# Kernel tuning notes

Measured on AMD Instinct MI355X. Metric: run time of the kernel, lower is better.

The kernel has to match this reference:

```python
import jax, jax.numpy as jnp
import numpy as np

N_TOKENS = 8192
D_MODEL = 1024
D_FF = 4096
N_EXPERTS = 8


def setup_inputs() -> dict:
    key = jax.random.key(0)
    ks = jax.random.split(key, 5)
    scale_in = 1.0 / np.sqrt(D_MODEL)
    x = jax.random.normal(ks[0], (N_TOKENS, D_MODEL), dtype=jnp.float32)
    gate_w = jax.random.normal(ks[1], (D_MODEL, N_EXPERTS), dtype=jnp.float32) * scale_in
    gate_b = jnp.zeros((N_EXPERTS,), dtype=jnp.float32)
    expert_w = jax.random.normal(ks[2], (N_EXPERTS, D_MODEL, D_FF), dtype=jnp.float32) * scale_in
    expert_b = jnp.zeros((N_EXPERTS, D_FF), dtype=jnp.float32)
    return {"x": x, "gate_w": gate_w, "gate_b": gate_b, "expert_w": expert_w, "expert_b": expert_b}


def reference(x, gate_w, gate_b, expert_w, expert_b):
    # Gate: [N, E] logits -> softmax -> top-1 expert per token
    gate_logits = x @ gate_w + gate_b
    gate_probs = jax.nn.softmax(gate_logits, axis=-1)
    top1 = jnp.argmax(gate_probs, axis=-1)  # [N], == argsort(...)[:, -1]

    # Dense all-expert compute, as in the original: [E, N, d_ff]
    expert_outputs = jnp.einsum('nd,edf->enf', x, expert_w) + expert_b[:, None, :]

    # Gather each token's top-1 expert output: [N, d_ff]
    selected = expert_outputs[top1, jnp.arange(x.shape[0])]
    return selected
```

## Files before the change

### kernel.cpp

```cpp
#include <hip/hip_runtime.h>


#define N_TOKENS 8192
#define D_MODEL  1024
#define D_FF     4096
#define N_EXPERTS 8

#define BM 128
#define BN 128
#define BK 64
#define NKT (D_MODEL / BK)
#define MT_MAX (N_TOKENS / BM + N_EXPERTS)
#define NTILES (D_FF / BN)
#define GATE_BLOCKS (N_TOKENS / 4)
#define WCONV_BLOCKS ((D_FF / 64) * (D_MODEL / 64) * N_EXPERTS)

typedef float  floatx4 __attribute__((ext_vector_type(4)));
typedef short  short8  __attribute__((ext_vector_type(8)));

__device__ __forceinline__ unsigned short f2bf(float f) {
    union { float f; unsigned u; } a; a.f = f;
    return (unsigned short)((a.u + 0x7fffu + ((a.u >> 16) & 1u)) >> 16);
}

#define GLDS(gp, lp) __builtin_amdgcn_global_load_lds( \
    (const __attribute__((address_space(1))) unsigned int*)(const void*)(gp), \
    (__attribute__((address_space(3))) unsigned int*)(void*)(lp), 16, 0, 0)

#define WST 68
__global__ __launch_bounds__(256) void prep_kernel(
    const float* __restrict__ x, const float* __restrict__ gw,
    const float* __restrict__ gb, const float* __restrict__ ew,
    unsigned short* __restrict__ xb, unsigned short* __restrict__ wt,
    int* __restrict__ top1)
{
    if (blockIdx.x < GATE_BLOCKS) {
        int wave = threadIdx.x >> 6;
        int l    = threadIdx.x & 63;
        int n = blockIdx.x * 4 + wave;
        const float4* xr = (const float4*)(x + (size_t)n * D_MODEL);
        float acc[N_EXPERTS];
#pragma unroll
        for (int e = 0; e < N_EXPERTS; ++e) acc[e] = 0.f;
#pragma unroll
        for (int j = 0; j < 4; ++j) {
            int d4 = j * 64 + l;
            float4 v = xr[d4];
            float vv[4] = { v.x, v.y, v.z, v.w };
#pragma unroll
            for (int t = 0; t < 4; ++t) {
                const float4* g = (const float4*)(gw + (size_t)(d4 * 4 + t) * N_EXPERTS);
                float4 g0 = g[0], g1 = g[1];
                acc[0] += vv[t] * g0.x; acc[1] += vv[t] * g0.y;
                acc[2] += vv[t] * g0.z; acc[3] += vv[t] * g0.w;
                acc[4] += vv[t] * g1.x; acc[5] += vv[t] * g1.y;
                acc[6] += vv[t] * g1.z; acc[7] += vv[t] * g1.w;
            }
            union { unsigned short us[4]; uint2 u; } pk;
            pk.us[0] = f2bf(v.x); pk.us[1] = f2bf(v.y);
            pk.us[2] = f2bf(v.z); pk.us[3] = f2bf(v.w);
            ((uint2*)(xb + (size_t)n * D_MODEL))[d4] = pk.u;
        }
#pragma unroll
        for (int e = 0; e < N_EXPERTS; ++e)
            for (int off = 32; off > 0; off >>= 1)
                acc[e] += __shfl_down(acc[e], off);
        if (l == 0) {
            float best = acc[0] + gb[0]; int be = 0;
#pragma unroll
            for (int e = 1; e < N_EXPERTS; ++e) {
                float v = acc[e] + gb[e];
                if (v > best) { best = v; be = e; }
            }
            top1[n] = be;
        }
    } else {
        __shared__ unsigned short tt[64 * WST];
        int b  = blockIdx.x - GATE_BLOCKS;
        int f0 = (b & 63) * 64;
        int d0 = ((b >> 6) & 15) * 64;
        int e  = b >> 10;
        int t  = threadIdx.x;
        const float* we = ew + (size_t)e * D_MODEL * D_FF + (size_t)d0 * D_FF + f0;
        int fg = (t & 15) * 4;
        int dg = (t >> 4) * 4;
        unsigned short v[4][4];
#pragma unroll
        for (int j = 0; j < 4; ++j) {
            float4 r = *(const float4*)(we + (size_t)(dg + j) * D_FF + fg);
            v[0][j] = f2bf(r.x); v[1][j] = f2bf(r.y);
            v[2][j] = f2bf(r.z); v[3][j] = f2bf(r.w);
        }
#pragma unroll
        for (int i = 0; i < 4; ++i) {
            union { unsigned short us[4]; uint2 u; } pk;
            pk.us[0] = v[i][0]; pk.us[1] = v[i][1];
            pk.us[2] = v[i][2]; pk.us[3] = v[i][3];
            *(uint2*)&tt[(fg + i) * WST + dg] = pk.u;
        }
        __syncthreads();
        unsigned short* wte = wt + (size_t)e * D_FF * D_MODEL + (size_t)f0 * D_MODEL + d0;
        int fr = t >> 3;
        int dr = (t & 7) * 8;
#pragma unroll
        for (int p = 0; p < 2; ++p) {
            int f = fr + p * 32;
            uint2 a = *(const uint2*)&tt[f * WST + dr];
            uint2 c = *(const uint2*)&tt[f * WST + dr + 4];
            uint4 o; o.x = a.x; o.y = a.y; o.z = c.x; o.w = c.y;
            *(uint4*)(wte + (size_t)f * D_MODEL + dr) = o;
        }
    }
}

__global__ __launch_bounds__(1024) void route_kernel(
    const int* __restrict__ top1, int* __restrict__ tile_expert, int* __restrict__ list)
{
    __shared__ int wtot[16][N_EXPERTS];
    __shared__ int wbase[16][N_EXPERTS];
    __shared__ int pofs[N_EXPERTS];
    int t = threadIdx.x, wv = t >> 6, l = t & 63;

    for (int i = t; i < MT_MAX * BM; i += 1024) list[i] = -1;

    int e8[8];
    const int4* tp = (const int4*)(top1 + t * 8);
    int4 a = tp[0], b = tp[1];
    e8[0] = a.x; e8[1] = a.y; e8[2] = a.z; e8[3] = a.w;
    e8[4] = b.x; e8[5] = b.y; e8[6] = b.z; e8[7] = b.w;
    int c[N_EXPERTS], s[N_EXPERTS];
#pragma unroll
    for (int e = 0; e < N_EXPERTS; ++e) c[e] = 0;
#pragma unroll
    for (int j = 0; j < 8; ++j) c[e8[j]]++;
#pragma unroll
    for (int e = 0; e < N_EXPERTS; ++e) s[e] = c[e];
    for (int off = 1; off < 64; off <<= 1) {
#pragma unroll
        for (int e = 0; e < N_EXPERTS; ++e) {
            int v = __shfl_up(s[e], off);
            if (l >= off) s[e] += v;
        }
    }
    if (l == 63)
#pragma unroll
        for (int e = 0; e < N_EXPERTS; ++e) wtot[wv][e] = s[e];
    __syncthreads();
    if (t == 0) {
        int cnt[N_EXPERTS];
        for (int e = 0; e < N_EXPERTS; ++e) {
            cnt[e] = 0;
            for (int w = 0; w < 16; ++w) { wbase[w][e] = cnt[e]; cnt[e] += wtot[w][e]; }
        }
        int off = 0;
        for (int e = 0; e < N_EXPERTS; ++e) {
            pofs[e] = off;
            int ntl = (cnt[e] + BM - 1) / BM;
            for (int k = 0; k < ntl; ++k) tile_expert[off / BM + k] = e;
            off += ntl * BM;
        }
        for (int k = off / BM; k < MT_MAX; ++k) tile_expert[k] = -1;
    }
    __syncthreads();
    int base[N_EXPERTS];
#pragma unroll
    for (int e = 0; e < N_EXPERTS; ++e) base[e] = pofs[e] + wbase[wv][e] + s[e] - c[e];
#pragma unroll
    for (int j = 0; j < 8; ++j) {
        int e = e8[j];
        list[base[e]++] = t * 8 + j;
    }
}

__global__ __launch_bounds__(256) void gemm_kernel(
    const unsigned short* __restrict__ xb,
    const unsigned short* __restrict__ wt,
    const float* __restrict__ eb,
    const int* __restrict__ tile_expert,
    const int* __restrict__ list,
    float* __restrict__ out)
{
    int bid = blockIdx.x;
    int xcd = bid & 7, w = bid >> 3;
    int mt  = w >> 2;
    int nt  = (xcd << 2) | (w & 3);
    int e = tile_expert[mt];
    if (e < 0) return;
    int n0 = nt * BN;

    __shared__ unsigned short As[BM * BK];
    __shared__ unsigned short Bs[BN * BK];
    __shared__ int toks[BM];

    int tid = threadIdx.x;
    int lane = tid & 63, wave = tid >> 6;
    if (tid < BM) toks[tid] = list[mt * BM + tid];
    __syncthreads();

    const unsigned short* gA[4];
    const unsigned short* gB[4];
    const unsigned short* wbase = wt + (size_t)e * D_FF * D_MODEL;
#pragma unroll
    for (int i = 0; i < 4; ++i) {
        int s = wave * 256 + i * 64 + lane;
        int row = s >> 3, c8 = (s & 7) ^ (row & 7);
        int ta = toks[row]; if (ta < 0) ta = 0;
        gA[i] = xb + (size_t)ta * D_MODEL + c8 * 8;
        gB[i] = wbase + (size_t)(n0 + row) * D_MODEL + c8 * 8;
    }

    floatx4 acc[4][4];
#pragma unroll
    for (int mi = 0; mi < 4; ++mi)
#pragma unroll
        for (int ni = 0; ni < 4; ++ni)
            acc[mi][ni] = (floatx4){0.f, 0.f, 0.f, 0.f};

    int mw = (wave >> 1) * 64;
    int nw = (wave & 1) * 64;
    int q = lane >> 4, r = lane & 15;
    int xr = r & 7;
    int ra[4], rb[4];
#pragma unroll
    for (int i = 0; i < 4; ++i) { ra[i] = (mw + i * 16 + r) * 8; rb[i] = (nw + i * 16 + r) * 8; }

    for (int kt = 0; kt < NKT; ++kt) {
        int k0 = kt * BK;
#pragma unroll
        for (int i = 0; i < 4; ++i) GLDS(gA[i] + k0, &As[(wave * 256 + i * 64) * 8]);
#pragma unroll
        for (int i = 0; i < 4; ++i) GLDS(gB[i] + k0, &Bs[(wave * 256 + i * 64) * 8]);
        __syncthreads();
#pragma unroll
        for (int ks = 0; ks < 2; ++ks) {
            int cq = (ks * 4 + q) ^ xr;
            short8 af[4], bf[4];
#pragma unroll
            for (int mi = 0; mi < 4; ++mi)
                af[mi] = *(const short8*)&As[(ra[mi] + cq) * 8];
#pragma unroll
            for (int ni = 0; ni < 4; ++ni)
                bf[ni] = *(const short8*)&Bs[(rb[ni] + cq) * 8];
#pragma unroll
            for (int mi = 0; mi < 4; ++mi)
#pragma unroll
                for (int ni = 0; ni < 4; ++ni)
                    acc[mi][ni] = __builtin_amdgcn_mfma_f32_16x16x32_bf16(
                        af[mi], bf[ni], acc[mi][ni], 0, 0, 0);
        }
        __syncthreads();
    }

#pragma unroll
    for (int ni = 0; ni < 4; ++ni) {
        int f = n0 + nw + ni * 16 + r;
        float bias = eb[(size_t)e * D_FF + f];
#pragma unroll
        for (int mi = 0; mi < 4; ++mi) {
            int mbase = mw + mi * 16 + q * 4;
#pragma unroll
            for (int i = 0; i < 4; ++i) {
                int tok = toks[mbase + i];
                if (tok >= 0) out[(size_t)tok * D_FF + f] = acc[mi][ni][i] + bias;
            }
        }
    }
}

extern "C" void kernel_launch(void* const* d_in, const int* in_sizes, int n_in,
                              void* d_out, int out_size, void* d_ws, size_t ws_size,
                              hipStream_t stream) {
    const float* x  = (const float*)d_in[0];
    const float* gw = (const float*)d_in[1];
    const float* gb = (const float*)d_in[2];
    const float* ew = (const float*)d_in[3];
    const float* eb = (const float*)d_in[4];
    float* out = (float*)d_out;

    char* ws = (char*)d_ws;
    int* top1        = (int*)ws;
    int* tile_expert = (int*)(ws + 32768);
    int* list        = (int*)(ws + 36864);
    unsigned short* xb = (unsigned short*)(ws + 131072);
    unsigned short* wt = (unsigned short*)(ws + 131072 + (size_t)N_TOKENS * D_MODEL * 2);

    hipLaunchKernelGGL(prep_kernel, dim3(GATE_BLOCKS + WCONV_BLOCKS), dim3(256), 0, stream,
                       x, gw, gb, ew, xb, wt, top1);
    hipLaunchKernelGGL(route_kernel, dim3(1), dim3(1024), 0, stream,
                       top1, tile_expert, list);
    hipLaunchKernelGGL(gemm_kernel, dim3(MT_MAX * NTILES), dim3(256), 0, stream,
                       xb, wt, eb, tile_expert, list, out);
}
```

Before: 441.9 us.

## Double-buffer LDS tiles to prefetch two K-steps ahead in expert GEMM

Splits the A and B shared-memory tiles into two buffers and issues the global-to-LDS loads for tile kt+2 right after computing tile kt, using vmcnt waits and raw barriers instead of __syncthreads. The aim is to hide global memory latency behind the MFMA work, which the single-buffered load-sync-compute loop leaves exposed. It doubles LDS usage to about 64KB per block, which can lower occupancy, and it relies on hand-written waitcnt counts being correct.

```diff
diff --git a/kernel.cpp b/kernel.cpp
--- a/kernel.cpp
+++ b/kernel.cpp
@@ -188,8 +188,8 @@
     if (e < 0) return;
     int n0 = nt * BN;
 
-    __shared__ unsigned short As[BM * BK];
-    __shared__ unsigned short Bs[BN * BK];
+    __shared__ unsigned short As[2][BM * BK];
+    __shared__ unsigned short Bs[2][BN * BK];
     __shared__ int toks[BM];
 
     int tid = threadIdx.x;
@@ -209,6 +209,16 @@
         gB[i] = wbase + (size_t)(n0 + row) * D_MODEL + c8 * 8;
     }
 
+    auto stage = [&](int b, int kt) {
+        int k0 = kt * BK;
+        unsigned short* ap = &As[b][0];
+        unsigned short* bp = &Bs[b][0];
+#pragma unroll
+        for (int i = 0; i < 4; ++i) GLDS(gA[i] + k0, ap + (size_t)(wave * 256 + i * 64) * 8);
+#pragma unroll
+        for (int i = 0; i < 4; ++i) GLDS(gB[i] + k0, bp + (size_t)(wave * 256 + i * 64) * 8);
+    };
+
     floatx4 acc[4][4];
 #pragma unroll
     for (int mi = 0; mi < 4; ++mi)
@@ -224,23 +234,26 @@
 #pragma unroll
     for (int i = 0; i < 4; ++i) { ra[i] = (mw + i * 16 + r) * 8; rb[i] = (nw + i * 16 + r) * 8; }
 
+    stage(0, 0);
+    stage(1, 1);
+    asm volatile("s_waitcnt vmcnt(8)" ::: "memory");
+    __builtin_amdgcn_s_barrier();
+    __builtin_amdgcn_sched_barrier(0);
+
     for (int kt = 0; kt < NKT; ++kt) {
-        int k0 = kt * BK;
-#pragma unroll
-        for (int i = 0; i < 4; ++i) GLDS(gA[i] + k0, &As[(wave * 256 + i * 64) * 8]);
-#pragma unroll
-        for (int i = 0; i < 4; ++i) GLDS(gB[i] + k0, &Bs[(wave * 256 + i * 64) * 8]);
-        __syncthreads();
+        int cur = kt & 1;
+        const unsigned short* Ac = &As[cur][0];
+        const unsigned short* Bc = &Bs[cur][0];
 #pragma unroll
         for (int ks = 0; ks < 2; ++ks) {
             int cq = (ks * 4 + q) ^ xr;
             short8 af[4], bf[4];
 #pragma unroll
             for (int mi = 0; mi < 4; ++mi)
-                af[mi] = *(const short8*)&As[(ra[mi] + cq) * 8];
+                af[mi] = *(const short8*)&Ac[(size_t)(ra[mi] + cq) * 8];
 #pragma unroll
             for (int ni = 0; ni < 4; ++ni)
-                bf[ni] = *(const short8*)&Bs[(rb[ni] + cq) * 8];
+                bf[ni] = *(const short8*)&Bc[(size_t)(rb[ni] + cq) * 8];
 #pragma unroll
             for (int mi = 0; mi < 4; ++mi)
 #pragma unroll
@@ -248,7 +261,16 @@
                     acc[mi][ni] = __builtin_amdgcn_mfma_f32_16x16x32_bf16(
                         af[mi], bf[ni], acc[mi][ni], 0, 0, 0);
         }
-        __syncthreads();
+        __builtin_amdgcn_sched_barrier(0);
+        __builtin_amdgcn_s_barrier();
+        if (kt + 2 < NKT) {
+            stage(cur, kt + 2);
+            asm volatile("s_waitcnt vmcnt(8)" ::: "memory");
+        } else {
+            asm volatile("s_waitcnt vmcnt(0)" ::: "memory");
+        }
+        __builtin_amdgcn_s_barrier();
+        __builtin_amdgcn_sched_barrier(0);
     }
 
 #pragma unroll
```

Measured after the change: 431.5 us. 1.02x faster.
